# Optimization experiments

Measured on AMD Instinct MI355X. Metric: run time of the kernel, lower is better.

The kernel has to match this reference:

```python
import jax, jax.numpy as jnp
import numpy as np

EMBED = 1024
HEADS = 16
HEAD_DIM = EMBED // HEADS


def setup_inputs() -> dict:
    key = jax.random.key(0)
    ks = jax.random.split(key, 9)
    B, S = 1, 4096
    scale = 1.0 / np.sqrt(EMBED)
    x = jax.random.normal(ks[0], (B, S, EMBED), dtype=jnp.float32)
    # nn.Linear weights stored as [out, in]; we store transposed [in, out] for x @ W
    Wq = jax.random.uniform(ks[1], (EMBED, EMBED), jnp.float32, -scale, scale)
    bq = jax.random.uniform(ks[2], (EMBED,), jnp.float32, -scale, scale)
    Wk = jax.random.uniform(ks[3], (EMBED, EMBED), jnp.float32, -scale, scale)
    bk = jax.random.uniform(ks[4], (EMBED,), jnp.float32, -scale, scale)
    Wv = jax.random.uniform(ks[5], (EMBED, EMBED), jnp.float32, -scale, scale)
    bv = jax.random.uniform(ks[6], (EMBED,), jnp.float32, -scale, scale)
    Wo = jax.random.uniform(ks[7], (EMBED, EMBED), jnp.float32, -scale, scale)
    bo = jax.random.uniform(ks[8], (EMBED,), jnp.float32, -scale, scale)
    return {"x": x, "Wq": Wq, "bq": bq, "Wk": Wk, "bk": bk,
            "Wv": Wv, "bv": bv, "Wo": Wo, "bo": bo}


def reference(x, Wq, bq, Wk, bk, Wv, bv, Wo, bo):
    B, S, E = x.shape
    H, D = HEADS, HEAD_DIM
    # projections
    Q = (x @ Wq + bq).reshape(B, S, H, D).transpose(0, 2, 1, 3)  # [B,H,S,D]
    K = (x @ Wk + bk).reshape(B, S, H, D).transpose(0, 2, 1, 3)
    V = (x @ Wv + bv).reshape(B, S, H, D).transpose(0, 2, 1, 3)
    # unfused attention: full [B,H,S,S] score matrix, matching the torch module
    scores = jnp.einsum('bhqd,bhkd->bhqk', Q, K) / jnp.sqrt(jnp.float32(D)).astype(x.dtype)
    probs = jax.nn.softmax(scores, axis=-1)
    out = jnp.einsum('bhqk,bhkd->bhqd', probs, V)  # [B,H,S,D]
    out = out.transpose(0, 2, 1, 3).reshape(B, S, E)
    return out @ Wo + bo
```

## Files before the change

### kernel.cpp

```cpp
#include <hip/hip_runtime.h>


constexpr int Sq = 4096;
constexpr int Ee = 1024;
constexpr int Hh = 16;
constexpr int Dh = 64;

typedef _Float16 half8 __attribute__((ext_vector_type(8)));
typedef _Float16 half4 __attribute__((ext_vector_type(4)));
typedef _Float16 half2t __attribute__((ext_vector_type(2)));
typedef float f32x4 __attribute__((ext_vector_type(4)));

union U8 { half8 v8; half2t h2[4]; };

__device__ __forceinline__ unsigned short f2h(float f) {
  _Float16 h = (_Float16)f;
  return *reinterpret_cast<unsigned short*>(&h);
}

__device__ __forceinline__ half2t pk(float a, float b) {
  return __builtin_bit_cast(half2t, __builtin_amdgcn_cvt_pkrtz(a, b));
}

__device__ __forceinline__ void gload16(const void* g, void* l) {
  __builtin_amdgcn_global_load_lds(
      (const __attribute__((address_space(1))) void*)g,
      (__attribute__((address_space(3))) void*)l, 16, 0, 0);
}

__global__ void k_prep(const float* __restrict__ x,
                       const float* __restrict__ Wq, const float* __restrict__ Wk,
                       const float* __restrict__ Wv, const float* __restrict__ Wo,
                       unsigned short* __restrict__ xb,
                       unsigned short* __restrict__ Wqt, unsigned short* __restrict__ Wkt,
                       unsigned short* __restrict__ Wvt, unsigned short* __restrict__ Wot) {
  int b = blockIdx.x, t = threadIdx.x;
  if (b < 4096) {
    int i = b * 256 + t;
    float4 v = reinterpret_cast<const float4*>(x)[i];
    ushort4 o;
    o.x = f2h(v.x); o.y = f2h(v.y); o.z = f2h(v.z); o.w = f2h(v.w);
    reinterpret_cast<ushort4*>(xb)[i] = o;
    return;
  }
  __shared__ unsigned short tile[64][65];
  int r = b - 4096;
  int wi = r >> 8, ti = r & 255;
  const float* W = (wi == 0) ? Wq : (wi == 1) ? Wk : (wi == 2) ? Wv : Wo;
  unsigned short* Wt = (wi == 0) ? Wqt : (wi == 1) ? Wkt : (wi == 2) ? Wvt : Wot;
  int kb = (ti & 15) * 64, nb = (ti >> 4) * 64;
  int r0 = t >> 4, c4 = (t & 15) * 4;
  for (int i = 0; i < 4; i++) {
    int row = r0 + i * 16;
    float4 v = *reinterpret_cast<const float4*>(W + (size_t)(kb + row) * Ee + nb + c4);
    tile[row][c4 + 0] = f2h(v.x); tile[row][c4 + 1] = f2h(v.y);
    tile[row][c4 + 2] = f2h(v.z); tile[row][c4 + 3] = f2h(v.w);
  }
  __syncthreads();
  for (int i = 0; i < 4; i++) {
    int nrow = r0 + i * 16;
    ushort4 o;
    o.x = tile[c4 + 0][nrow]; o.y = tile[c4 + 1][nrow];
    o.z = tile[c4 + 2][nrow]; o.w = tile[c4 + 3][nrow];
    *reinterpret_cast<ushort4*>(Wt + (size_t)(nb + nrow) * Ee + kb + c4) = o;
  }
}

template <bool TR>
__device__ __forceinline__ void gemm_kloop(
    const unsigned short* __restrict__ A, const unsigned short* __restrict__ Wt,
    unsigned short* Al, unsigned short* Bl,
    int m0, int n0, int t, int wm, int wn, int quad, int c, f32x4 (&acc)[4][4]) {
  auto stageAB = [&](int buf, int k0) {
#pragma unroll
    for (int i = 0; i < 4; i++) {
      int ch = i * 256 + t;
      int row = ch >> 3, kg = (ch & 7) ^ (row & 7);
      gload16(A + (size_t)(m0 + row) * 1024 + k0 + kg * 8, &Al[buf * 8192 + ch * 8]);
    }
#pragma unroll
    for (int i = 0; i < 4; i++) {
      int ch = i * 256 + t;
      int row = ch >> 3, kg = (ch & 7) ^ (row & 7);
      gload16(Wt + (size_t)(n0 + row) * 1024 + k0 + kg * 8, &Bl[buf * 8192 + ch * 8]);
    }
  };
  auto compute = [&](int cur) {
    const unsigned short* Ab = &Al[cur * 8192];
    const unsigned short* Bb = &Bl[cur * 8192];
#pragma unroll
    for (int ks = 0; ks < 2; ks++) {
      half8 af[4], bfr[4];
#pragma unroll
      for (int i = 0; i < 4; i++) {
        int row = wm * 64 + i * 16 + c;
        int kg = (quad + 4 * ks) ^ (row & 7);
        af[i] = *reinterpret_cast<const half8*>(&Ab[row * 64 + kg * 8]);
      }
#pragma unroll
      for (int j = 0; j < 4; j++) {
        int row = wn * 64 + j * 16 + c;
        int kg = (quad + 4 * ks) ^ (row & 7);
        bfr[j] = *reinterpret_cast<const half8*>(&Bb[row * 64 + kg * 8]);
      }
#pragma unroll
      for (int i = 0; i < 4; i++)
#pragma unroll
        for (int j = 0; j < 4; j++) {
          if (TR)
            acc[j][i] = __builtin_amdgcn_mfma_f32_16x16x32_f16(bfr[j], af[i], acc[j][i], 0, 0, 0);
          else
            acc[i][j] = __builtin_amdgcn_mfma_f32_16x16x32_f16(af[i], bfr[j], acc[i][j], 0, 0, 0);
        }
    }
  };
  stageAB(0, 0);
  stageAB(1, 64);
  for (int k0 = 0; k0 < 960; k0 += 64) {
    int cur = (k0 >> 6) & 1;
    asm volatile("s_waitcnt vmcnt(8)" ::: "memory");
    __builtin_amdgcn_s_barrier();
    __builtin_amdgcn_sched_barrier(0);
    compute(cur);
    __builtin_amdgcn_s_barrier();
    if (k0 < 896) stageAB(cur, k0 + 128);
  }
  asm volatile("s_waitcnt vmcnt(0)" ::: "memory");
  __builtin_amdgcn_s_barrier();
  __builtin_amdgcn_sched_barrier(0);
  compute(1);
}

__global__ __launch_bounds__(256) void k_gemm(
    const unsigned short* __restrict__ A,
    const unsigned short* __restrict__ W0, const unsigned short* __restrict__ W1,
    const unsigned short* __restrict__ W2,
    const float* __restrict__ b0, const float* __restrict__ b1, const float* __restrict__ b2,
    void* d0, void* d1, void* d2) {
  __shared__ __align__(16) unsigned short Al[2 * 128 * 64];
  __shared__ __align__(16) unsigned short Bl[2 * 128 * 64];
  int bid = blockIdx.x;
  int yp = bid & 7;
  int rest = bid >> 3;
  int xm = rest & 31;
  int z = rest >> 5;
  const unsigned short* Wt; const float* bias; void* dst;
  if (z == 0)      { Wt = W0; bias = b0; dst = d0; }
  else if (z == 1) { Wt = W1; bias = b1; dst = d1; }
  else             { Wt = W2; bias = b2; dst = d2; }

  int t = threadIdx.x;
  int w = t >> 6, L = t & 63, quad = L >> 4, c = L & 15;
  int m0 = xm * 128, n0 = yp * 128;
  int wm = w >> 1, wn = w & 1;

  f32x4 zero = {0.f, 0.f, 0.f, 0.f};
  f32x4 acc[4][4];
#pragma unroll
  for (int i = 0; i < 4; i++)
#pragma unroll
    for (int j = 0; j < 4; j++) acc[i][j] = zero;

  if (z < 2) gemm_kloop<true>(A, Wt, Al, Bl, m0, n0, t, wm, wn, quad, c, acc);
  else       gemm_kloop<false>(A, Wt, Al, Bl, m0, n0, t, wm, wn, quad, c, acc);

  if (z < 2) {
    float sc = (z == 0) ? 0.18033688011112042f : 1.0f;
    unsigned short* qk = (unsigned short*)dst;
#pragma unroll
    for (int j = 0; j < 4; j++) {
      int nb4 = n0 + wn * 64 + j * 16 + quad * 4;
      int hh = nb4 >> 6, d = nb4 & 63;
      f32x4 b4 = *reinterpret_cast<const f32x4*>(bias + nb4);
#pragma unroll
      for (int i = 0; i < 4; i++) {
        int s = m0 + wm * 64 + i * 16 + c;
        half4 hv;
#pragma unroll
        for (int r = 0; r < 4; r++) hv[r] = (_Float16)((acc[j][i][r] + b4[r]) * sc);
        *reinterpret_cast<half4*>(&qk[(size_t)hh * Sq * Dh + (size_t)s * Dh + d]) = hv;
      }
    }
    return;
  }
  unsigned short* Vt = (unsigned short*)dst;
#pragma unroll
  for (int j = 0; j < 4; j++) {
    int n = n0 + wn * 64 + j * 16 + c;
    int hh = n >> 6, d = n & 63;
    float bv = bias[n];
#pragma unroll
    for (int i = 0; i < 4; i++) {
      int pos = m0 + wm * 64 + (i >> 1) * 32 + quad * 8 + (i & 1) * 4;
      half4 hv;
#pragma unroll
      for (int r = 0; r < 4; r++) hv[r] = (_Float16)(acc[i][j][r] + bv);
      *reinterpret_cast<half4*>(&Vt[(size_t)hh * Dh * Sq + (size_t)d * Sq + pos]) = hv;
    }
  }
}

__global__ __launch_bounds__(256) void k_gemmO(
    const unsigned short* __restrict__ A, const unsigned short* __restrict__ Wt,
    const float* __restrict__ bias, float* __restrict__ out) {
  __shared__ __align__(16) unsigned short Al[2 * 64 * 64];
  __shared__ __align__(16) unsigned short Bl[2 * 128 * 64];
  int bid = blockIdx.x;
  int yp = bid & 7;
  int xm = bid >> 3;
  int t = threadIdx.x;
  int w = t >> 6, L = t & 63, quad = L >> 4, c = L & 15;
  int m0 = xm * 64, n0 = yp * 128;
  int wm = w & 1, wn = w >> 1;

  f32x4 zero = {0.f, 0.f, 0.f, 0.f};
  f32x4 acc[4][2];
#pragma unroll
  for (int j = 0; j < 4; j++)
#pragma unroll
    for (int i = 0; i < 2; i++) acc[j][i] = zero;

  auto stageAB = [&](int buf, int k0) {
#pragma unroll
    for (int i = 0; i < 2; i++) {
      int ch = i * 256 + t;
      int row = ch >> 3, kg = (ch & 7) ^ (row & 7);
      gload16(A + (size_t)(m0 + row) * 1024 + k0 + kg * 8, &Al[buf * 4096 + ch * 8]);
    }
#pragma unroll
    for (int i = 0; i < 4; i++) {
      int ch = i * 256 + t;
      int row = ch >> 3, kg = (ch & 7) ^ (row & 7);
      gload16(Wt + (size_t)(n0 + row) * 1024 + k0 + kg * 8, &Bl[buf * 8192 + ch * 8]);
    }
  };
  auto compute = [&](int cur) {
    const unsigned short* Ab = &Al[cur * 4096];
    const unsigned short* Bb = &Bl[cur * 8192];
#pragma unroll
    for (int ks = 0; ks < 2; ks++) {
      half8 af[2], bfr[4];
#pragma unroll
      for (int i = 0; i < 2; i++) {
        int row = wm * 32 + i * 16 + c;
        int kg = (quad + 4 * ks) ^ (row & 7);
        af[i] = *reinterpret_cast<const half8*>(&Ab[row * 64 + kg * 8]);
      }
#pragma unroll
      for (int j = 0; j < 4; j++) {
        int row = wn * 64 + j * 16 + c;
        int kg = (quad + 4 * ks) ^ (row & 7);
        bfr[j] = *reinterpret_cast<const half8*>(&Bb[row * 64 + kg * 8]);
      }
#pragma unroll
      for (int j = 0; j < 4; j++)
#pragma unroll
        for (int i = 0; i < 2; i++)
          acc[j][i] = __builtin_amdgcn_mfma_f32_16x16x32_f16(bfr[j], af[i], acc[j][i], 0, 0, 0);
    }
  };
  stageAB(0, 0);
  stageAB(1, 64);
  for (int k0 = 0; k0 < 960; k0 += 64) {
    int cur = (k0 >> 6) & 1;
    asm volatile("s_waitcnt vmcnt(6)" ::: "memory");
    __builtin_amdgcn_s_barrier();
    __builtin_amdgcn_sched_barrier(0);
    compute(cur);
    __builtin_amdgcn_s_barrier();
    if (k0 < 896) stageAB(cur, k0 + 128);
  }
  asm volatile("s_waitcnt vmcnt(0)" ::: "memory");
  __builtin_amdgcn_s_barrier();
  __builtin_amdgcn_sched_barrier(0);
  compute(1);

#pragma unroll
  for (int j = 0; j < 4; j++) {
    int nb4 = n0 + wn * 64 + j * 16 + quad * 4;
    f32x4 b4 = *reinterpret_cast<const f32x4*>(bias + nb4);
#pragma unroll
    for (int i = 0; i < 2; i++) {
      int s = m0 + wm * 32 + i * 16 + c;
      f32x4 v = acc[j][i] + b4;
      *reinterpret_cast<f32x4*>(out + (size_t)s * 1024 + nb4) = v;
    }
  }
}

__global__ __launch_bounds__(256, 2) void k_attn(
    const unsigned short* __restrict__ Q, const unsigned short* __restrict__ K,
    const unsigned short* __restrict__ Vt, unsigned short* __restrict__ O) {
  __shared__ __align__(16) unsigned short SM[32768];
  int t = threadIdx.x;
  int w = t >> 6, L = t & 63, quad = L >> 4, c = L & 15;
  int wl = w & 1, par = w >> 1;
  int h = blockIdx.y, qb = blockIdx.x;
  const unsigned short* Qh = Q + (size_t)h * Sq * Dh;
  const unsigned short* Kh = K + (size_t)h * Sq * Dh;
  const unsigned short* Vth = Vt + (size_t)h * Dh * Sq;

  half8 qf[4][2];
#pragma unroll
  for (int qg = 0; qg < 4; qg++) {
    int qrow = qb * 128 + wl * 64 + qg * 16 + c;
#pragma unroll
    for (int ks = 0; ks < 2; ks++)
      qf[qg][ks] = *reinterpret_cast<const half8*>(Qh + (size_t)qrow * Dh + ks * 32 + quad * 8);
  }

  f32x4 zero = {0.f, 0.f, 0.f, 0.f};
  f32x4 o[4][4];
  f32x4 l[4];
#pragma unroll
  for (int qg = 0; qg < 4; qg++) {
    l[qg] = zero;
#pragma unroll
    for (int dt = 0; dt < 4; dt++) o[qg][dt] = zero;
  }
  half8 ones8;
#pragma unroll
  for (int j = 0; j < 8; j++) ones8[j] = (_Float16)1.0f;

  int koff[2][4], voff[4][2];
#pragma unroll
  for (int ks = 0; ks < 2; ks++)
#pragma unroll
    for (int nt = 0; nt < 4; nt++) {
      int row = nt * 16 + c;
      koff[ks][nt] = par * 4096 + row * 64 + (((ks * 4 + quad) ^ (row & 7)) * 8);
    }
#pragma unroll
  for (int dt = 0; dt < 4; dt++)
#pragma unroll
    for (int n2 = 0; n2 < 2; n2++) {
      int row = dt * 16 + c;
      voff[dt][n2] = (2 + par) * 4096 + row * 64 + (((n2 * 4 + quad) ^ (row & 7)) * 8);
    }

  const unsigned short* KgB[2];
  const unsigned short* VgB[2];
#pragma unroll
  for (int i = 0; i < 2; i++) {
    int ch = i * 256 + t;
    int row = ch >> 3, kg = (ch & 7) ^ (row & 7);
    KgB[i] = Kh + row * Dh + kg * 8;
    VgB[i] = Vth + (size_t)row * Sq + kg * 8;
  }

  auto stage = [&](int bufo, int tb) {
#pragma unroll
    for (int p2 = 0; p2 < 2; p2++) {
#pragma unroll
      for (int i = 0; i < 2; i++)
        gload16(KgB[i] + (size_t)(tb + p2) * 4096, &SM[bufo + p2 * 4096 + (i * 256 + t) * 8]);
#pragma unroll
      for (int i = 0; i < 2; i++)
        gload16(VgB[i] + (size_t)(tb + p2) * 64, &SM[bufo + (2 + p2) * 4096 + (i * 256 + t) * 8]);
    }
  };

  stage(0, 0);

  auto body = [&](int BUFOFF) {
    half8 pB[4][2];
#pragma unroll
    for (int h2 = 0; h2 < 2; h2++) {
      f32x4 st[2][4];
      __builtin_amdgcn_s_setprio(1);
#pragma unroll
      for (int nt = 0; nt < 4; nt++) {
        half8 kfv = *reinterpret_cast<const half8*>(&SM[koff[0][nt] + BUFOFF]);
        st[0][nt] = __builtin_amdgcn_mfma_f32_16x16x32_f16(kfv, qf[2 * h2 + 0][0], zero, 0, 0, 0);
        st[1][nt] = __builtin_amdgcn_mfma_f32_16x16x32_f16(kfv, qf[2 * h2 + 1][0], zero, 0, 0, 0);
      }
#pragma unroll
      for (int nt = 0; nt < 4; nt++) {
        half8 kfv = *reinterpret_cast<const half8*>(&SM[koff[1][nt] + BUFOFF]);
        st[0][nt] = __builtin_amdgcn_mfma_f32_16x16x32_f16(kfv, qf[2 * h2 + 0][1], st[0][nt], 0, 0, 0);
        st[1][nt] = __builtin_amdgcn_mfma_f32_16x16x32_f16(kfv, qf[2 * h2 + 1][1], st[1][nt], 0, 0, 0);
      }
      __builtin_amdgcn_s_setprio(0);
#pragma unroll
      for (int q2 = 0; q2 < 2; q2++)
#pragma unroll
        for (int n2 = 0; n2 < 2; n2++) {
          U8 u;
          u.h2[0] = pk(__builtin_amdgcn_exp2f(st[q2][2 * n2][0]), __builtin_amdgcn_exp2f(st[q2][2 * n2][1]));
          u.h2[1] = pk(__builtin_amdgcn_exp2f(st[q2][2 * n2][2]), __builtin_amdgcn_exp2f(st[q2][2 * n2][3]));
          u.h2[2] = pk(__builtin_amdgcn_exp2f(st[q2][2 * n2 + 1][0]), __builtin_amdgcn_exp2f(st[q2][2 * n2 + 1][1]));
          u.h2[3] = pk(__builtin_amdgcn_exp2f(st[q2][2 * n2 + 1][2]), __builtin_amdgcn_exp2f(st[q2][2 * n2 + 1][3]));
          pB[2 * h2 + q2][n2] = u.v8;
          l[2 * h2 + q2] = __builtin_amdgcn_mfma_f32_16x16x32_f16(ones8, u.v8, l[2 * h2 + q2], 0, 0, 0);
        }
    }
    __builtin_amdgcn_s_setprio(1);
#pragma unroll
    for (int dt = 0; dt < 4; dt++)
#pragma unroll
      for (int n2 = 0; n2 < 2; n2++) {
        half8 vv = *reinterpret_cast<const half8*>(&SM[voff[dt][n2] + BUFOFF]);
        o[0][dt] = __builtin_amdgcn_mfma_f32_16x16x32_f16(vv, pB[0][n2], o[0][dt], 0, 0, 0);
        o[1][dt] = __builtin_amdgcn_mfma_f32_16x16x32_f16(vv, pB[1][n2], o[1][dt], 0, 0, 0);
        o[2][dt] = __builtin_amdgcn_mfma_f32_16x16x32_f16(vv, pB[2][n2], o[2][dt], 0, 0, 0);
        o[3][dt] = __builtin_amdgcn_mfma_f32_16x16x32_f16(vv, pB[3][n2], o[3][dt], 0, 0, 0);
      }
    __builtin_amdgcn_s_setprio(0);
  };

  for (int ob2 = 0; ob2 < 16; ob2++) {
    __syncthreads();
    stage(16384, 4 * ob2 + 2);
    body(0);
    __syncthreads();
    if (ob2 < 15) stage(0, 4 * ob2 + 4);
    body(16384);
  }

  __syncthreads();
  float* cb = (float*)SM;
  if (par == 1) {
#pragma unroll
    for (int qg = 0; qg < 4; qg++)
#pragma unroll
      for (int dt = 0; dt < 4; dt++)
        *reinterpret_cast<f32x4*>(cb + ((wl * 17 + qg * 4 + dt) * 64 + L) * 4) = o[qg][dt];
    f32x4 lv = {l[0][0], l[1][0], l[2][0], l[3][0]};
    *reinterpret_cast<f32x4*>(cb + ((wl * 17 + 16) * 64 + L) * 4) = lv;
  }
  __syncthreads();
  if (par == 0) {
#pragma unroll
    for (int qg = 0; qg < 4; qg++)
#pragma unroll
      for (int dt = 0; dt < 4; dt++)
        o[qg][dt] += *reinterpret_cast<const f32x4*>(cb + ((wl * 17 + qg * 4 + dt) * 64 + L) * 4);
    f32x4 lv = *reinterpret_cast<const f32x4*>(cb + ((wl * 17 + 16) * 64 + L) * 4);
#pragma unroll
    for (int qg = 0; qg < 4; qg++) {
      float inv = 1.f / (l[qg][0] + lv[qg]);
      int q = qb * 128 + wl * 64 + qg * 16 + c;
#pragma unroll
      for (int dt = 0; dt < 4; dt++) {
        half4 hv;
#pragma unroll
        for (int r = 0; r < 4; r++) hv[r] = (_Float16)(o[qg][dt][r] * inv);
        *reinterpret_cast<half4*>(&O[(size_t)q * 1024 + h * 64 + dt * 16 + quad * 4]) = hv;
      }
    }
  }
}

extern "C" void kernel_launch(void* const* d_in, const int* in_sizes, int n_in,
                              void* d_out, int out_size, void* d_ws, size_t ws_size,
                              hipStream_t stream) {
  const float* x  = (const float*)d_in[0];
  const float* Wq = (const float*)d_in[1];
  const float* bq = (const float*)d_in[2];
  const float* Wk = (const float*)d_in[3];
  const float* bk = (const float*)d_in[4];
  const float* Wv = (const float*)d_in[5];
  const float* bv = (const float*)d_in[6];
  const float* Wo = (const float*)d_in[7];
  const float* bo = (const float*)d_in[8];

  char* ws = (char*)d_ws;
  const size_t MB = 1u << 20;
  unsigned short* xb  = (unsigned short*)(ws);
  unsigned short* Wqt = (unsigned short*)(ws + 8 * MB);
  unsigned short* Wkt = (unsigned short*)(ws + 10 * MB);
  unsigned short* Wvt = (unsigned short*)(ws + 12 * MB);
  unsigned short* Wot = (unsigned short*)(ws + 14 * MB);
  unsigned short* Qb  = (unsigned short*)(ws + 16 * MB);
  unsigned short* Kb  = (unsigned short*)(ws + 24 * MB);
  unsigned short* Vtg = (unsigned short*)(ws + 32 * MB);
  unsigned short* Ob  = (unsigned short*)(ws + 40 * MB);

  k_prep<<<5120, 256, 0, stream>>>(x, Wq, Wk, Wv, Wo, xb, Wqt, Wkt, Wvt, Wot);
  k_gemm<<<768, 256, 0, stream>>>(xb, Wqt, Wkt, Wvt, bq, bk, bv,
                                  (void*)Qb, (void*)Kb, (void*)Vtg);
  k_attn<<<dim3(32, 16), 256, 0, stream>>>(Qb, Kb, Vtg, Ob);
  k_gemmO<<<512, 256, 0, stream>>>(Ob, Wot, bo, (float*)d_out);
}
```

Before: 220.9 us.

## Fuse Q/K/V projections into one block sharing the staged x tile

The QKV projection kernel now computes all three outputs in a single 512-thread block. Each block stages one x tile plus three weight tiles per k-step, so the x tile is loaded once instead of three times across separate blocks. The grid shrinks from 768 to 256 blocks, and each wave covers a 64x32 sub-tile for each of the three projections. Shared memory grows to about 128KB per block, so occupancy is lower, and 256 blocks may underfill the 256 CUs on the device.

After: 212.6 us. 1.04x faster.

```diff
diff --git a/kernel.cpp b/kernel.cpp
--- a/kernel.cpp
+++ b/kernel.cpp
@@ -66,54 +66,86 @@
   }
 }
 
-template <bool TR>
-__device__ __forceinline__ void gemm_kloop(
-    const unsigned short* __restrict__ A, const unsigned short* __restrict__ Wt,
-    unsigned short* Al, unsigned short* Bl,
-    int m0, int n0, int t, int wm, int wn, int quad, int c, f32x4 (&acc)[4][4]) {
+__global__ __launch_bounds__(512, 2) void k_gemm(
+    const unsigned short* __restrict__ A,
+    const unsigned short* __restrict__ W0, const unsigned short* __restrict__ W1,
+    const unsigned short* __restrict__ W2,
+    const float* __restrict__ b0, const float* __restrict__ b1, const float* __restrict__ b2,
+    void* d0, void* d1, void* d2) {
+  __shared__ __align__(16) unsigned short Al[2 * 8192];
+  __shared__ __align__(16) unsigned short Bl[2 * 3 * 8192];
+  int bid = blockIdx.x;
+  int yp = bid & 7;
+  int xm = bid >> 3;
+  int m0 = xm * 128, n0 = yp * 128;
+
+  int t = threadIdx.x;
+  int w = t >> 6, L = t & 63, quad = L >> 4, c = L & 15;
+  int wm = w >> 2, wn = w & 3;
+
+  const unsigned short* Wz[3] = {W0, W1, W2};
+
+  f32x4 zero = {0.f, 0.f, 0.f, 0.f};
+  f32x4 acc[3][4][2];
+#pragma unroll
+  for (int z = 0; z < 3; z++)
+#pragma unroll
+    for (int a = 0; a < 4; a++)
+#pragma unroll
+      for (int b = 0; b < 2; b++) acc[z][a][b] = zero;
+
   auto stageAB = [&](int buf, int k0) {
 #pragma unroll
-    for (int i = 0; i < 4; i++) {
-      int ch = i * 256 + t;
+    for (int i = 0; i < 2; i++) {
+      int ch = i * 512 + t;
       int row = ch >> 3, kg = (ch & 7) ^ (row & 7);
       gload16(A + (size_t)(m0 + row) * 1024 + k0 + kg * 8, &Al[buf * 8192 + ch * 8]);
     }
 #pragma unroll
-    for (int i = 0; i < 4; i++) {
-      int ch = i * 256 + t;
-      int row = ch >> 3, kg = (ch & 7) ^ (row & 7);
-      gload16(Wt + (size_t)(n0 + row) * 1024 + k0 + kg * 8, &Bl[buf * 8192 + ch * 8]);
-    }
-  };
+    for (int z = 0; z < 3; z++)
+#pragma unroll
+      for (int i = 0; i < 2; i++) {
+        int ch = i * 512 + t;
+        int row = ch >> 3, kg = (ch & 7) ^ (row & 7);
+        gload16(Wz[z] + (size_t)(n0 + row) * 1024 + k0 + kg * 8,
+                &Bl[(buf * 3 + z) * 8192 + ch * 8]);
+      }
+  };
+
   auto compute = [&](int cur) {
     const unsigned short* Ab = &Al[cur * 8192];
-    const unsigned short* Bb = &Bl[cur * 8192];
 #pragma unroll
     for (int ks = 0; ks < 2; ks++) {
-      half8 af[4], bfr[4];
-#pragma unroll
-      for (int i = 0; i < 4; i++) {
-        int row = wm * 64 + i * 16 + c;
+      half8 af[4];
+#pragma unroll
+      for (int a = 0; a < 4; a++) {
+        int row = wm * 64 + a * 16 + c;
         int kg = (quad + 4 * ks) ^ (row & 7);
-        af[i] = *reinterpret_cast<const half8*>(&Ab[row * 64 + kg * 8]);
-      }
-#pragma unroll
-      for (int j = 0; j < 4; j++) {
-        int row = wn * 64 + j * 16 + c;
-        int kg = (quad + 4 * ks) ^ (row & 7);
-        bfr[j] = *reinterpret_cast<const half8*>(&Bb[row * 64 + kg * 8]);
-      }
-#pragma unroll
-      for (int i = 0; i < 4; i++)
-#pragma unroll
-        for (int j = 0; j < 4; j++) {
-          if (TR)
-            acc[j][i] = __builtin_amdgcn_mfma_f32_16x16x32_f16(bfr[j], af[i], acc[j][i], 0, 0, 0);
-          else
-            acc[i][j] = __builtin_amdgcn_mfma_f32_16x16x32_f16(af[i], bfr[j], acc[i][j], 0, 0, 0);
+        af[a] = *reinterpret_cast<const half8*>(&Ab[row * 64 + kg * 8]);
+      }
+#pragma unroll
+      for (int z = 0; z < 3; z++) {
+        const unsigned short* Bb = &Bl[(cur * 3 + z) * 8192];
+        half8 bfr[2];
+#pragma unroll
+        for (int b = 0; b < 2; b++) {
+          int row = wn * 32 + b * 16 + c;
+          int kg = (quad + 4 * ks) ^ (row & 7);
+          bfr[b] = *reinterpret_cast<const half8*>(&Bb[row * 64 + kg * 8]);
         }
-    }
-  };
+#pragma unroll
+        for (int a = 0; a < 4; a++)
+#pragma unroll
+          for (int b = 0; b < 2; b++) {
+            if (z < 2)
+              acc[z][a][b] = __builtin_amdgcn_mfma_f32_16x16x32_f16(bfr[b], af[a], acc[z][a][b], 0, 0, 0);
+            else
+              acc[z][a][b] = __builtin_amdgcn_mfma_f32_16x16x32_f16(af[a], bfr[b], acc[z][a][b], 0, 0, 0);
+          }
+      }
+    }
+  };
+
   stageAB(0, 0);
   stageAB(1, 64);
   for (int k0 = 0; k0 < 960; k0 += 64) {
@@ -129,73 +161,46 @@
   __builtin_amdgcn_s_barrier();
   __builtin_amdgcn_sched_barrier(0);
   compute(1);
-}
-
-__global__ __launch_bounds__(256) void k_gemm(
-    const unsigned short* __restrict__ A,
-    const unsigned short* __restrict__ W0, const unsigned short* __restrict__ W1,
-    const unsigned short* __restrict__ W2,
-    const float* __restrict__ b0, const float* __restrict__ b1, const float* __restrict__ b2,
-    void* d0, void* d1, void* d2) {
-  __shared__ __align__(16) unsigned short Al[2 * 128 * 64];
-  __shared__ __align__(16) unsigned short Bl[2 * 128 * 64];
-  int bid = blockIdx.x;
-  int yp = bid & 7;
-  int rest = bid >> 3;
-  int xm = rest & 31;
-  int z = rest >> 5;
-  const unsigned short* Wt; const float* bias; void* dst;
-  if (z == 0)      { Wt = W0; bias = b0; dst = d0; }
-  else if (z == 1) { Wt = W1; bias = b1; dst = d1; }
-  else             { Wt = W2; bias = b2; dst = d2; }
-
-  int t = threadIdx.x;
-  int w = t >> 6, L = t & 63, quad = L >> 4, c = L & 15;
-  int m0 = xm * 128, n0 = yp * 128;
-  int wm = w >> 1, wn = w & 1;
-
-  f32x4 zero = {0.f, 0.f, 0.f, 0.f};
-  f32x4 acc[4][4];
-#pragma unroll
-  for (int i = 0; i < 4; i++)
-#pragma unroll
-    for (int j = 0; j < 4; j++) acc[i][j] = zero;
-
-  if (z < 2) gemm_kloop<true>(A, Wt, Al, Bl, m0, n0, t, wm, wn, quad, c, acc);
-  else       gemm_kloop<false>(A, Wt, Al, Bl, m0, n0, t, wm, wn, quad, c, acc);
-
-  if (z < 2) {
-    float sc = (z == 0) ? 0.18033688011112042f : 1.0f;
-    unsigned short* qk = (unsigned short*)dst;
-#pragma unroll
-    for (int j = 0; j < 4; j++) {
-      int nb4 = n0 + wn * 64 + j * 16 + quad * 4;
-      int hh = nb4 >> 6, d = nb4 & 63;
-      f32x4 b4 = *reinterpret_cast<const f32x4*>(bias + nb4);
-#pragma unroll
-      for (int i = 0; i < 4; i++) {
-        int s = m0 + wm * 64 + i * 16 + c;
+
+  {
+    unsigned short* qk0 = (unsigned short*)d0;
+    unsigned short* qk1 = (unsigned short*)d1;
+#pragma unroll
+    for (int z = 0; z < 2; z++) {
+      float sc = (z == 0) ? 0.18033688011112042f : 1.0f;
+      const float* bias = (z == 0) ? b0 : b1;
+      unsigned short* qk = (z == 0) ? qk0 : qk1;
+#pragma unroll
+      for (int b = 0; b < 2; b++) {
+        int nb4 = n0 + wn * 32 + b * 16 + quad * 4;
+        int hh = nb4 >> 6, d = nb4 & 63;
+        f32x4 b4 = *reinterpret_cast<const f32x4*>(bias + nb4);
+#pragma unroll
+        for (int a = 0; a < 4; a++) {
+          int s = m0 + wm * 64 + a * 16 + c;
+          half4 hv;
+#pragma unroll
+          for (int r = 0; r < 4; r++) hv[r] = (_Float16)((acc[z][a][b][r] + b4[r]) * sc);
+          *reinterpret_cast<half4*>(&qk[(size_t)hh * Sq * Dh + (size_t)s * Dh + d]) = hv;
+        }
+      }
+    }
+  }
+  {
+    unsigned short* Vt = (unsigned short*)d2;
+#pragma unroll
+    for (int b = 0; b < 2; b++) {
+      int n = n0 + wn * 32 + b * 16 + c;
+      int hh = n >> 6, d = n & 63;
+      float bv = b2[n];
+#pragma unroll
+      for (int a = 0; a < 4; a++) {
+        int pos = m0 + wm * 64 + (a >> 1) * 32 + quad * 8 + (a & 1) * 4;
         half4 hv;
 #pragma unroll
-        for (int r = 0; r < 4; r++) hv[r] = (_Float16)((acc[j][i][r] + b4[r]) * sc);
-        *reinterpret_cast<half4*>(&qk[(size_t)hh * Sq * Dh + (size_t)s * Dh + d]) = hv;
-      }
-    }
-    return;
-  }
-  unsigned short* Vt = (unsigned short*)dst;
-#pragma unroll
-  for (int j = 0; j < 4; j++) {
-    int n = n0 + wn * 64 + j * 16 + c;
-    int hh = n >> 6, d = n & 63;
-    float bv = bias[n];
-#pragma unroll
-    for (int i = 0; i < 4; i++) {
-      int pos = m0 + wm * 64 + (i >> 1) * 32 + quad * 8 + (i & 1) * 4;
-      half4 hv;
-#pragma unroll
-      for (int r = 0; r < 4; r++) hv[r] = (_Float16)(acc[i][j][r] + bv);
-      *reinterpret_cast<half4*>(&Vt[(size_t)hh * Dh * Sq + (size_t)d * Sq + pos]) = hv;
+        for (int r = 0; r < 4; r++) hv[r] = (_Float16)(acc[2][a][b][r] + bv);
+        *reinterpret_cast<half4*>(&Vt[(size_t)hh * Dh * Sq + (size_t)d * Sq + pos]) = hv;
+      }
     }
   }
 }
@@ -477,7 +482,7 @@
   unsigned short* Ob  = (unsigned short*)(ws + 40 * MB);
 
   k_prep<<<5120, 256, 0, stream>>>(x, Wq, Wk, Wv, Wo, xb, Wqt, Wkt, Wvt, Wot);
-  k_gemm<<<768, 256, 0, stream>>>(xb, Wqt, Wkt, Wvt, bq, bk, bv,
+  k_gemm<<<256, 512, 0, stream>>>(xb, Wqt, Wkt, Wvt, bq, bk, bv,
                                   (void*)Qb, (void*)Kb, (void*)Vtg);
   k_attn<<<dim3(32, 16), 256, 0, stream>>>(Qb, Kb, Vtg, Ob);
   k_gemmO<<<512, 256, 0, stream>>>(Ob, Wot, bo, (float*)d_out);
```
